# Kernel optimization log

Hardware: AMD Instinct MI355X
Metric: run time of the kernel (lower is better)

The kernel has to match this reference:

```python
import jax, jax.numpy as jnp
import numpy as np

N, D, R, E = 50000, 128, 16, 1600000


def rgcn_conv(x, W, root, bias, src, dst, rel):
    """PyG-style RGCNConv (aggr='mean', root weight + bias).
    out[i] = x[i] @ root + bias + sum_r mean_{j in N_r(i)} x[j] @ W_r
    Aggregate-then-transform: segment-mean per (relation, dst) then contract with W.
    """
    n, d = x.shape
    seg = rel * n + dst  # combined (relation, dst-node) segment id
    msg_sum = jax.ops.segment_sum(x[src], seg, num_segments=R * n).reshape(R, n, d)
    cnt = jax.ops.segment_sum(jnp.ones_like(src, dtype=x.dtype), seg, num_segments=R * n).reshape(R, n, 1)
    msg = msg_sum / jnp.maximum(cnt, 1.0)  # mean aggregation (0 when no edges)
    return jnp.einsum('rnd,rde->ne', msg, W) + x @ root + bias


def setup_inputs() -> dict:
    key = jax.random.key(0)
    ks = jax.random.split(key, 9)
    x = jax.random.normal(ks[0], (N, D), dtype=jnp.float32)
    edge_index = jax.random.randint(ks[1], (2, E), 0, N, dtype=jnp.int64)
    edge_type = jax.random.randint(ks[2], (E,), 0, R, dtype=jnp.int64)
    s = 1.0 / np.sqrt(D)
    W1 = jax.random.normal(ks[3], (R, D, D), dtype=jnp.float32) * s
    root1 = jax.random.normal(ks[4], (D, D), dtype=jnp.float32) * s
    b1 = jnp.zeros((D,), dtype=jnp.float32)
    W2 = jax.random.normal(ks[5], (R, D, D), dtype=jnp.float32) * s
    root2 = jax.random.normal(ks[6], (D, D), dtype=jnp.float32) * s
    b2 = jnp.zeros((D,), dtype=jnp.float32)
    return {"x": x, "edge_index": edge_index, "edge_type": edge_type,
            "W1": W1, "root1": root1, "b1": b1,
            "W2": W2, "root2": root2, "b2": b2}


def reference(x, edge_index, edge_type, W1, root1, b1, W2, root2, b2):
    src, dst = edge_index[0], edge_index[1]
    # layer 1: RGCN -> ReLU -> Dropout (identity in eval mode)
    h = jax.nn.relu(rgcn_conv(x, W1, root1, b1, src, dst, edge_type))
    # layer 2: RGCN -> ReLU
    h = jax.nn.relu(rgcn_conv(h, W2, root2, b2, src, dst, edge_type))
    return h
```

## Files before the change

kernel.cpp:

```cpp
#include <hip/hip_runtime.h>


#define ND 128
#define NR 16
#define KPB 4096

typedef __attribute__((ext_vector_type(8))) short bf16x8;
typedef __attribute__((ext_vector_type(4))) float f32x4;
typedef __attribute__((ext_vector_type(4))) unsigned int u32x4;

__device__ __forceinline__ unsigned short f2b(float f) {
    unsigned u = __float_as_uint(f);
    u += 0x7FFFu + ((u >> 16) & 1u);
    return (unsigned short)(u >> 16);
}

__global__ __launch_bounds__(256) void coarse_hist(
    const int* __restrict__ dst, const int* __restrict__ rel,
    int* __restrict__ coarse_cnt, int E, int N, int NBK)
{
    __shared__ int h[1024];
    const int t = threadIdx.x;
    for (int i = t; i < NBK; i += 256) h[i] = 0;
    __syncthreads();
#pragma unroll
    for (int q = 0; q < 16; ++q) {
        int e = blockIdx.x * KPB + q * 256 + t;
        if (e < E) {
            int key = rel[e] * N + dst[e];
            atomicAdd(&h[key >> 12], 1);
        }
    }
    __syncthreads();
    for (int i = t; i < NBK; i += 256)
        if (h[i]) atomicAdd(&coarse_cnt[i], h[i]);
}

__global__ __launch_bounds__(1024) void coarse_scan(
    const int* __restrict__ coarse_cnt, int* __restrict__ cscan,
    int* __restrict__ coarse_cursor, int NBK, int E)
{
    __shared__ int sdata[1024];
    const int t = threadIdx.x;
    int v = (t < NBK) ? coarse_cnt[t] : 0;
    sdata[t] = v;
    __syncthreads();
    for (int off = 1; off < 1024; off <<= 1) {
        int tmp = (t >= off) ? sdata[t - off] : 0;
        __syncthreads();
        sdata[t] += tmp;
        __syncthreads();
    }
    if (t < NBK) {
        int excl = sdata[t] - v;
        cscan[t] = excl;
        coarse_cursor[t] = excl;
    }
    if (t == 0) cscan[NBK] = E;
}

__global__ __launch_bounds__(256) void fillA(
    const int* __restrict__ src, const int* __restrict__ dst,
    const int* __restrict__ rel, int* __restrict__ coarse_cursor,
    uint2* __restrict__ coarse_buf, int E, int N, int NBK)
{
    __shared__ uint2 pairs[KPB];
    __shared__ int h[1024];
    const int t = threadIdx.x;
    for (int i = t; i < NBK; i += 256) h[i] = 0;
    __syncthreads();
#pragma unroll
    for (int q = 0; q < 16; ++q) {
        int e = blockIdx.x * KPB + q * 256 + t;
        unsigned key = 0xFFFFFFFFu, sv = 0;
        if (e < E) {
            key = (unsigned)(rel[e] * N + dst[e]);
            sv = (unsigned)src[e];
            atomicAdd(&h[key >> 12], 1);
        }
        pairs[q * 256 + t] = make_uint2(sv, key);
    }
    __syncthreads();
    for (int i = t; i < NBK; i += 256) {
        int c = h[i];
        h[i] = c ? atomicAdd(&coarse_cursor[i], c) : 0;
    }
    __syncthreads();
#pragma unroll
    for (int q = 0; q < 16; ++q) {
        uint2 p = pairs[q * 256 + t];
        if (p.y != 0xFFFFFFFFu) {
            int pos = atomicAdd(&h[p.y >> 12], 1);
            coarse_buf[pos] = p;
        }
    }
}

__global__ __launch_bounds__(256) void fillB(
    const uint2* __restrict__ coarse_buf, const int* __restrict__ cscan,
    int* __restrict__ seg_off, float* __restrict__ cnt_inv,
    int* __restrict__ sorted_src, int M, int E, int NBK)
{
    __shared__ int cnt[KPB];
    __shared__ int w[256];
    const int t = threadIdx.x;
    const int b = blockIdx.x;
    const int kbase = b << 12;
    const int nkeys = min(KPB, M - kbase);
    const int r0 = cscan[b], r1 = cscan[b + 1];

    for (int i = t; i < KPB; i += 256) cnt[i] = 0;
    __syncthreads();
    for (int e = r0 + t; e < r1; e += 256)
        atomicAdd(&cnt[coarse_buf[e].y - kbase], 1);
    __syncthreads();
    for (int i = t; i < nkeys; i += 256)
        cnt_inv[kbase + i] = 1.0f / fmaxf((float)cnt[i], 1.0f);
    int s = 0;
#pragma unroll
    for (int j = 0; j < 16; ++j) s += cnt[t * 16 + j];
    w[t] = s;
    __syncthreads();
    for (int off = 1; off < 256; off <<= 1) {
        int tmp = (t >= off) ? w[t - off] : 0;
        __syncthreads();
        w[t] += tmp;
        __syncthreads();
    }
    int run = r0 + w[t] - s;
#pragma unroll
    for (int j = 0; j < 16; ++j) {
        int i = t * 16 + j;
        int c = cnt[i];
        cnt[i] = run;
        if (i < nkeys) seg_off[kbase + i] = run;
        run += c;
    }
    if (b == NBK - 1 && t == 0) seg_off[M] = E;
    __syncthreads();
    for (int e = r0 + t; e < r1; e += 256) {
        uint2 p = coarse_buf[e];
        int pos = atomicAdd(&cnt[p.y - kbase], 1);
        sorted_src[pos] = (int)p.x;
    }
}

__global__ __launch_bounds__(256) void conv_x_kernel(
    const float* __restrict__ x, unsigned short* __restrict__ xb, int n4)
{
    int i = blockIdx.x * 256 + threadIdx.x;
    if (i >= n4) return;
    float4 v = ((const float4*)x)[i];
    uint2 o;
    o.x = (unsigned)f2b(v.x) | ((unsigned)f2b(v.y) << 16);
    o.y = (unsigned)f2b(v.z) | ((unsigned)f2b(v.w) << 16);
    ((uint2*)xb)[i] = o;
}

__global__ __launch_bounds__(256) void conv_w_kernel(
    const float* __restrict__ W, const float* __restrict__ root,
    unsigned short* __restrict__ Wt)
{
    int t = blockIdx.x * 256 + threadIdx.x;
    if (t >= 17 * 2048) return;
    int mat = t >> 11;
    int f = t & 2047;
    int lane = f & 63;
    int ctkt = f >> 6;
    int kt = ctkt >> 3;
    int ct = ctkt & 7;
    int n = ct * 16 + (lane & 15);
    int k = kt * 32 + (lane >> 4) * 8;
    const float* s = (mat < 16) ? (W + (size_t)mat * 16384) : root;
    uint4 o;
    o.x = (unsigned)f2b(s[(size_t)(k + 0) * ND + n]) | ((unsigned)f2b(s[(size_t)(k + 1) * ND + n]) << 16);
    o.y = (unsigned)f2b(s[(size_t)(k + 2) * ND + n]) | ((unsigned)f2b(s[(size_t)(k + 3) * ND + n]) << 16);
    o.z = (unsigned)f2b(s[(size_t)(k + 4) * ND + n]) | ((unsigned)f2b(s[(size_t)(k + 5) * ND + n]) << 16);
    o.w = (unsigned)f2b(s[(size_t)(k + 6) * ND + n]) | ((unsigned)f2b(s[(size_t)(k + 7) * ND + n]) << 16);
    *(uint4*)(Wt + (size_t)t * 8) = o;
}

__global__ __launch_bounds__(256) void gather_mean(
    const unsigned short* __restrict__ A,
    const int* __restrict__ seg_off,
    const int* __restrict__ sorted_src,
    const float* __restrict__ cnt_inv,
    unsigned short* __restrict__ msg,
    int N, int r0, int ccN)
{
    int g = blockIdx.x * 16 + (threadIdx.x >> 4);
    if (g >= ccN) return;
    int l = threadIdx.x & 15;
    int s = r0 * N + g;
    int b0 = seg_off[s], e1 = seg_off[s + 1];
    float a0 = 0.f, a1 = 0.f, a2 = 0.f, a3 = 0.f, a4 = 0.f, a5 = 0.f, a6 = 0.f, a7 = 0.f;
    int e = b0;
    for (; e + 2 <= e1; e += 2) {
        int s0 = sorted_src[e];
        int s1 = sorted_src[e + 1];
        uint4 u0 = *(const uint4*)(A + (size_t)s0 * ND + l * 8);
        uint4 u1 = *(const uint4*)(A + (size_t)s1 * ND + l * 8);
        a0 += __uint_as_float(u0.x << 16); a1 += __uint_as_float(u0.x & 0xFFFF0000u);
        a2 += __uint_as_float(u0.y << 16); a3 += __uint_as_float(u0.y & 0xFFFF0000u);
        a4 += __uint_as_float(u0.z << 16); a5 += __uint_as_float(u0.z & 0xFFFF0000u);
        a6 += __uint_as_float(u0.w << 16); a7 += __uint_as_float(u0.w & 0xFFFF0000u);
        a0 += __uint_as_float(u1.x << 16); a1 += __uint_as_float(u1.x & 0xFFFF0000u);
        a2 += __uint_as_float(u1.y << 16); a3 += __uint_as_float(u1.y & 0xFFFF0000u);
        a4 += __uint_as_float(u1.z << 16); a5 += __uint_as_float(u1.z & 0xFFFF0000u);
        a6 += __uint_as_float(u1.w << 16); a7 += __uint_as_float(u1.w & 0xFFFF0000u);
    }
    if (e < e1) {
        int s0 = sorted_src[e];
        uint4 u0 = *(const uint4*)(A + (size_t)s0 * ND + l * 8);
        a0 += __uint_as_float(u0.x << 16); a1 += __uint_as_float(u0.x & 0xFFFF0000u);
        a2 += __uint_as_float(u0.y << 16); a3 += __uint_as_float(u0.y & 0xFFFF0000u);
        a4 += __uint_as_float(u0.z << 16); a5 += __uint_as_float(u0.z & 0xFFFF0000u);
        a6 += __uint_as_float(u0.w << 16); a7 += __uint_as_float(u0.w & 0xFFFF0000u);
    }
    float inv = cnt_inv[s];
    u32x4 o;
    o.x = (unsigned)f2b(a0 * inv) | ((unsigned)f2b(a1 * inv) << 16);
    o.y = (unsigned)f2b(a2 * inv) | ((unsigned)f2b(a3 * inv) << 16);
    o.z = (unsigned)f2b(a4 * inv) | ((unsigned)f2b(a5 * inv) << 16);
    o.w = (unsigned)f2b(a6 * inv) | ((unsigned)f2b(a7 * inv) << 16);
    __builtin_nontemporal_store(o, (u32x4*)(msg + (size_t)g * ND + l * 8));
}

__global__ __launch_bounds__(256) void gemm_mfma(
    const unsigned short* __restrict__ msg,
    const unsigned short* __restrict__ xb,
    const unsigned short* __restrict__ Wt,
    const float* __restrict__ bias,
    float* __restrict__ acc_buf,
    unsigned short* __restrict__ out_bf,
    float* __restrict__ out_f32,
    int N, int c0, int cc, int include_root, int load_acc, int finalize)
{
    __shared__ __align__(16) unsigned short Bs[2048 * 8];
    const int tid = threadIdx.x;
    const int lane = tid & 63;
    const int wv = tid >> 6;
    const int quad = lane >> 4;
    const int l16 = lane & 15;
    const int m0 = blockIdx.x * 64 + wv * 16;
    const int arow = m0 + l16;

    f32x4 acc[8];
    if (load_acc) {
#pragma unroll
        for (int ct = 0; ct < 8; ++ct)
#pragma unroll
            for (int rg = 0; rg < 4; ++rg) {
                int r = m0 + quad * 4 + rg;
                acc[ct][rg] = (r < N) ? acc_buf[(size_t)r * ND + ct * 16 + l16] : 0.f;
            }
    } else {
#pragma unroll
        for (int ct = 0; ct < 8; ++ct) { f32x4 z = {0.f, 0.f, 0.f, 0.f}; acc[ct] = z; }
    }

    for (int rel = include_root ? -1 : 0; rel < cc; ++rel) {
        const unsigned short* A = (rel < 0) ? xb : msg + (size_t)rel * N * ND;
        const int mat = (rel < 0) ? 16 : (c0 + rel);
        const uint4* Bsrc = (const uint4*)(Wt + (size_t)mat * 2048 * 8);

        bf16x8 a[4];
#pragma unroll
        for (int kt = 0; kt < 4; ++kt) {
            bf16x8 z = {0, 0, 0, 0, 0, 0, 0, 0};
            const bf16x8* ap = (const bf16x8*)(A + (size_t)arow * ND + kt * 32 + quad * 8);
            if (arow < N) {
                a[kt] = (rel < 0) ? *ap : __builtin_nontemporal_load(ap);
            } else {
                a[kt] = z;
            }
        }

        __syncthreads();
#pragma unroll
        for (int i = 0; i < 8; ++i)
            ((uint4*)Bs)[tid + i * 256] = Bsrc[tid + i * 256];
        __syncthreads();

#pragma unroll
        for (int kt = 0; kt < 4; ++kt) {
#pragma unroll
            for (int ct = 0; ct < 8; ++ct) {
                bf16x8 b = *(const bf16x8*)(Bs + (size_t)((kt * 8 + ct) * 64 + lane) * 8);
                acc[ct] = __builtin_amdgcn_mfma_f32_16x16x32_bf16(a[kt], b, acc[ct], 0, 0, 0);
            }
        }
    }

    if (!finalize) {
#pragma unroll
        for (int ct = 0; ct < 8; ++ct)
#pragma unroll
            for (int rg = 0; rg < 4; ++rg) {
                int r = m0 + quad * 4 + rg;
                if (r < N) acc_buf[(size_t)r * ND + ct * 16 + l16] = acc[ct][rg];
            }
    } else {
#pragma unroll
        for (int ct = 0; ct < 8; ++ct) {
            float bb = bias[ct * 16 + l16];
#pragma unroll
            for (int rg = 0; rg < 4; ++rg) {
                int r = m0 + quad * 4 + rg;
                if (r < N) {
                    float v = fmaxf(acc[ct][rg] + bb, 0.f);
                    if (out_bf) out_bf[(size_t)r * ND + ct * 16 + l16] = f2b(v);
                    else        __builtin_nontemporal_store(v, &out_f32[(size_t)r * ND + ct * 16 + l16]);
                }
            }
        }
    }
}

extern "C" void kernel_launch(void* const* d_in, const int* in_sizes, int n_in,
                              void* d_out, int out_size, void* d_ws, size_t ws_size,
                              hipStream_t stream) {
    const float* x     = (const float*)d_in[0];
    const int*   eidx  = (const int*)d_in[1];
    const int*   etype = (const int*)d_in[2];
    const float* W1    = (const float*)d_in[3];
    const float* root1 = (const float*)d_in[4];
    const float* b1    = (const float*)d_in[5];
    const float* W2    = (const float*)d_in[6];
    const float* root2 = (const float*)d_in[7];
    const float* b2    = (const float*)d_in[8];
    float* out = (float*)d_out;

    const int N = in_sizes[0] / ND;
    const int E = in_sizes[2];
    const int M = NR * N;
    const int NBK = (M + KPB - 1) / KPB;

    const int* src = eidx;
    const int* dst = eidx + E;

    char* p = (char*)d_ws;
    auto carve = [&](size_t bytes) { char* q = p; p += (bytes + 255) & ~(size_t)255; return q; };
    unsigned short* h_bf    = (unsigned short*)carve((size_t)N * ND * 2);
    unsigned short* x_bf    = (unsigned short*)carve((size_t)N * ND * 2);
    unsigned short* Wt1     = (unsigned short*)carve((size_t)17 * 2048 * 8 * 2);
    unsigned short* Wt2     = (unsigned short*)carve((size_t)17 * 2048 * 8 * 2);
    int*   seg_off          = (int*)  carve((size_t)(M + 1) * 4);
    float* cnt_inv          = (float*)carve((size_t)M * 4);
    int*   sorted_src       = (int*)  carve((size_t)E * 4);
    int*   coarse_cnt       = (int*)  carve(1024 * 4);
    int*   cscan            = (int*)  carve(1025 * 4);
    int*   coarse_cursor    = (int*)  carve(1024 * 4);

    size_t fixed = (size_t)(p - (char*)d_ws);
    size_t remain = (ws_size > fixed) ? ws_size - fixed : 0;
    size_t chunk_bytes = (size_t)N * ND * 2;
    size_t acc_bytes   = (size_t)N * ND * 4;
    int C = 2;
    if (remain >= 16 * chunk_bytes + 512) C = 16;
    else if (remain >= 8 * chunk_bytes + acc_bytes + 512) C = 8;
    else if (remain >= 4 * chunk_bytes + acc_bytes + 512) C = 4;
    uint2* coarse_buf       = (uint2*)p;
    unsigned short* msg     = (unsigned short*)carve((size_t)C * chunk_bytes);
    float* acc              = (float*)((C < 16) ? carve(acc_bytes) : (char*)p);

    const int eb4 = (E + KPB - 1) / KPB;
    const int gemm_blocks = (N + 63) / 64;

    hipMemsetAsync(coarse_cnt, 0, 1024 * 4, stream);
    coarse_hist<<<eb4, 256, 0, stream>>>(dst, etype, coarse_cnt, E, N, NBK);
    coarse_scan<<<1, 1024, 0, stream>>>(coarse_cnt, cscan, coarse_cursor, NBK, E);
    fillA<<<eb4, 256, 0, stream>>>(src, dst, etype, coarse_cursor, coarse_buf, E, N, NBK);
    fillB<<<NBK, 256, 0, stream>>>(coarse_buf, cscan, seg_off, cnt_inv, sorted_src, M, E, NBK);

    conv_x_kernel<<<((N * ND / 4) + 255) / 256, 256, 0, stream>>>(x, x_bf, N * ND / 4);
    conv_w_kernel<<<(17 * 2048 + 255) / 256, 256, 0, stream>>>(W1, root1, Wt1);
    conv_w_kernel<<<(17 * 2048 + 255) / 256, 256, 0, stream>>>(W2, root2, Wt2);

    for (int layer = 0; layer < 2; ++layer) {
        const unsigned short* A  = (layer == 0) ? x_bf : h_bf;
        const unsigned short* Wt = (layer == 0) ? Wt1  : Wt2;
        const float* biasp       = (layer == 0) ? b1   : b2;

        for (int c0 = 0; c0 < NR; c0 += C) {
            int cc = (NR - c0 < C) ? (NR - c0) : C;
            int ccN = cc * N;
            gather_mean<<<(ccN + 15) / 16, 256, 0, stream>>>(
                A, seg_off, sorted_src, cnt_inv, msg, N, c0, ccN);
            int fin = (c0 + cc == NR) ? 1 : 0;
            gemm_mfma<<<gemm_blocks, 256, 0, stream>>>(
                msg, A, Wt, biasp, acc,
                (fin && layer == 0) ? h_bf : (unsigned short*)nullptr,
                (fin && layer == 1) ? out : (float*)nullptr,
                N, c0, cc, c0 == 0 ? 1 : 0, c0 > 0 ? 1 : 0, fin);
        }
    }
}
```

Baseline: 527.8 us.

## Software-pipeline relation loop by prefetching next A fragments and weights into registers

The per-relation GEMM loop now loads the next relation's message fragments and weight tile into registers before running the current relation's MFMAs, then commits the weights to shared memory afterwards. This is meant to hide global-memory latency behind the matrix math instead of stalling at the start of each relation. It costs extra registers for the prefetch buffers (8 uint4 plus 4 bf16x8 per thread), which may reduce occupancy.

```diff
diff --git a/kernel.cpp b/kernel.cpp
--- a/kernel.cpp
+++ b/kernel.cpp
@@ -259,36 +259,60 @@
         for (int ct = 0; ct < 8; ++ct) { f32x4 z = {0.f, 0.f, 0.f, 0.f}; acc[ct] = z; }
     }
 
-    for (int rel = include_root ? -1 : 0; rel < cc; ++rel) {
-        const unsigned short* A = (rel < 0) ? xb : msg + (size_t)rel * N * ND;
-        const int mat = (rel < 0) ? 16 : (c0 + rel);
-        const uint4* Bsrc = (const uint4*)(Wt + (size_t)mat * 2048 * 8);
-
-        bf16x8 a[4];
+    const int rel0 = include_root ? -1 : 0;
+    const bf16x8 zfrag = {0, 0, 0, 0, 0, 0, 0, 0};
+    bf16x8 aC[4];
+
+    {
+        const unsigned short* A0 = (rel0 < 0) ? xb : msg;
+        const int mat0 = (rel0 < 0) ? 16 : c0;
+        const uint4* B0 = (const uint4*)(Wt + (size_t)mat0 * 2048 * 8);
+        uint4 br[8];
+#pragma unroll
+        for (int i = 0; i < 8; ++i) br[i] = B0[tid + i * 256];
 #pragma unroll
         for (int kt = 0; kt < 4; ++kt) {
-            bf16x8 z = {0, 0, 0, 0, 0, 0, 0, 0};
-            const bf16x8* ap = (const bf16x8*)(A + (size_t)arow * ND + kt * 32 + quad * 8);
-            if (arow < N) {
-                a[kt] = (rel < 0) ? *ap : __builtin_nontemporal_load(ap);
-            } else {
-                a[kt] = z;
+            const bf16x8* ap = (const bf16x8*)(A0 + (size_t)arow * ND + kt * 32 + quad * 8);
+            if (arow < N) aC[kt] = (rel0 < 0) ? *ap : __builtin_nontemporal_load(ap);
+            else          aC[kt] = zfrag;
+        }
+#pragma unroll
+        for (int i = 0; i < 8; ++i) ((uint4*)Bs)[tid + i * 256] = br[i];
+    }
+    __syncthreads();
+
+    for (int rel = rel0; rel < cc; ++rel) {
+        const int nrel = rel + 1;
+        bf16x8 aN[4];
+        uint4 bN[8];
+        if (nrel < cc) {
+            const unsigned short* An = msg + (size_t)nrel * (size_t)N * ND;
+            const uint4* Bn = (const uint4*)(Wt + (size_t)(c0 + nrel) * 2048 * 8);
+#pragma unroll
+            for (int i = 0; i < 8; ++i) bN[i] = Bn[tid + i * 256];
+#pragma unroll
+            for (int kt = 0; kt < 4; ++kt) {
+                const bf16x8* ap = (const bf16x8*)(An + (size_t)arow * ND + kt * 32 + quad * 8);
+                aN[kt] = (arow < N) ? __builtin_nontemporal_load(ap) : zfrag;
             }
         }
-
-        __syncthreads();
-#pragma unroll
-        for (int i = 0; i < 8; ++i)
-            ((uint4*)Bs)[tid + i * 256] = Bsrc[tid + i * 256];
-        __syncthreads();
 
 #pragma unroll
         for (int kt = 0; kt < 4; ++kt) {
 #pragma unroll
             for (int ct = 0; ct < 8; ++ct) {
                 bf16x8 b = *(const bf16x8*)(Bs + (size_t)((kt * 8 + ct) * 64 + lane) * 8);
-                acc[ct] = __builtin_amdgcn_mfma_f32_16x16x32_bf16(a[kt], b, acc[ct], 0, 0, 0);
+                acc[ct] = __builtin_amdgcn_mfma_f32_16x16x32_bf16(aC[kt], b, acc[ct], 0, 0, 0);
             }
+        }
+
+        if (nrel < cc) {
+            __syncthreads();
+#pragma unroll
+            for (int i = 0; i < 8; ++i) ((uint4*)Bs)[tid + i * 256] = bN[i];
+#pragma unroll
+            for (int kt = 0; kt < 4; ++kt) aC[kt] = aN[kt];
+            __syncthreads();
         }
     }
 
```

Result: slower. 746.7 us (+41.5%).
